# Kernel optimization log

Hardware: AMD Instinct MI355X
Metric: run time of the kernel (lower is better)

## Reference

```python
import jax, jax.numpy as jnp
import numpy as np

NUM_CODES = 100000
DIM = 64
N_VISITS = 16384
MAX_CODES = 64


def setup_inputs() -> dict:
    key = jax.random.key(0)
    k1, k2 = jax.random.split(key)
    # ids in [-5, NUM_CODES): negatives act as padding (original filters ids >= 0)
    code_ids = jax.random.randint(k1, (N_VISITS, MAX_CODES), -5, NUM_CODES, dtype=jnp.int64)
    emb_weight = jax.random.normal(k2, (NUM_CODES, DIM), dtype=jnp.float32)
    return {"code_ids": code_ids, "emb_weight": emb_weight}


def reference(code_ids, emb_weight):
    # mask of valid (non-negative) code ids per visit
    mask = code_ids >= 0                                  # [N, C] bool
    safe_ids = jnp.where(mask, code_ids, 0)               # clamp padding to 0 for gather
    x = emb_weight[safe_ids]                              # [N, C, D] gather
    maskf = mask.astype(emb_weight.dtype)
    sums = jnp.einsum('ncd,nc->nd', x, maskf)             # masked sum over codes
    counts = maskf.sum(axis=1, keepdims=True)             # [N, 1]
    # mean over valid ids; visits with zero valid ids -> zero vector
    out = sums / jnp.maximum(counts, 1.0)
    return jnp.where(counts > 0, out, 0.0)
```

## Files before the change

kernel.cpp:

```cpp
#include <hip/hip_runtime.h>

#define N_VISITS  16384
#define MAX_CODES 64
#define DIM       64

__global__ __launch_bounds__(256) void visit_mean_kernel(
    const int* __restrict__ code_ids,
    const float* __restrict__ emb,
    float* __restrict__ out)
{
    const int wave_in_block = threadIdx.x >> 6;
    const int lane = threadIdx.x & 63;
    const int visit = blockIdx.x * 4 + wave_in_block;
    if (visit >= N_VISITS) return;

    const int my_id = code_ids[visit * MAX_CODES + lane];

    const unsigned long long valid = __ballot(my_id >= 0);
    const int count = __popcll(valid);

    float sum = 0.0f;

    #pragma unroll
    for (int j0 = 0; j0 < MAX_CODES; j0 += 16) {
        float v[16];
        float m[16];
        #pragma unroll
        for (int k = 0; k < 16; ++k) {
            const int idj  = __shfl(my_id, j0 + k, 64);
            const int safe = (idj >= 0) ? idj : 0;
            m[k] = (idj >= 0) ? 1.0f : 0.0f;
            v[k] = emb[(size_t)safe * DIM + lane];
        }
        #pragma unroll
        for (int k = 0; k < 16; ++k) {
            sum = fmaf(m[k], v[k], sum);
        }
    }

    const float scale = (count > 0) ? (1.0f / (float)count) : 0.0f;
    out[visit * DIM + lane] = sum * scale;
}

extern "C" void kernel_launch(void* const* d_in, const int* in_sizes, int n_in,
                              void* d_out, int out_size, void* d_ws, size_t ws_size,
                              hipStream_t stream) {
    const int*   code_ids = (const int*)d_in[0];
    const float* emb      = (const float*)d_in[1];
    float*       out      = (float*)d_out;

    const int waves_per_block = 4;
    const int grid = N_VISITS / waves_per_block;
    visit_mean_kernel<<<grid, 256, 0, stream>>>(code_ids, emb, out);
}
```

Baseline: 100.9 us.

## Vectorize embedding gathers with float4 loads and cross-lane reduction

Each wave now processes four embedding rows at a time: lanes are split into four groups of 16, and each lane loads a float4 from its assigned row. Sixteen gathered rows per lane are accumulated, and the four partial sums are combined with xor shuffles before 16 lanes write float4 outputs. This replaces 64 scalar gather loads per lane with 16 wider loads, cutting the number of memory instructions and giving more loads in flight. The cost is more registers for the 16 float4 values and an added shuffle reduction stage. The bounds check on the visit index is also removed.

```diff
diff --git a/kernel.cpp b/kernel.cpp
--- a/kernel.cpp
+++ b/kernel.cpp
@@ -12,34 +12,56 @@
     const int wave_in_block = threadIdx.x >> 6;
     const int lane = threadIdx.x & 63;
     const int visit = blockIdx.x * 4 + wave_in_block;
-    if (visit >= N_VISITS) return;
 
-    const int my_id = code_ids[visit * MAX_CODES + lane];
+    const int r = lane >> 4;
+    const int t = lane & 15;
 
+    const int my_id = code_ids[(size_t)visit * MAX_CODES + lane];
     const unsigned long long valid = __ballot(my_id >= 0);
     const int count = __popcll(valid);
 
-    float sum = 0.0f;
-
+    int ids[16];
     #pragma unroll
-    for (int j0 = 0; j0 < MAX_CODES; j0 += 16) {
-        float v[16];
-        float m[16];
-        #pragma unroll
-        for (int k = 0; k < 16; ++k) {
-            const int idj  = __shfl(my_id, j0 + k, 64);
-            const int safe = (idj >= 0) ? idj : 0;
-            m[k] = (idj >= 0) ? 1.0f : 0.0f;
-            v[k] = emb[(size_t)safe * DIM + lane];
-        }
-        #pragma unroll
-        for (int k = 0; k < 16; ++k) {
-            sum = fmaf(m[k], v[k], sum);
-        }
+    for (int j = 0; j < 16; ++j) {
+        ids[j] = __shfl(my_id, 4 * j + r, 64);
     }
 
-    const float scale = (count > 0) ? (1.0f / (float)count) : 0.0f;
-    out[visit * DIM + lane] = sum * scale;
+    float4 v[16];
+    #pragma unroll
+    for (int j = 0; j < 16; ++j) {
+        const int id   = ids[j];
+        const int safe = (id >= 0) ? id : 0;
+        v[j] = *((const float4*)(emb + (size_t)safe * DIM) + t);
+    }
+
+    float4 acc = make_float4(0.f, 0.f, 0.f, 0.f);
+    #pragma unroll
+    for (int j = 0; j < 16; ++j) {
+        const float m = (ids[j] >= 0) ? 1.0f : 0.0f;
+        acc.x = fmaf(m, v[j].x, acc.x);
+        acc.y = fmaf(m, v[j].y, acc.y);
+        acc.z = fmaf(m, v[j].z, acc.z);
+        acc.w = fmaf(m, v[j].w, acc.w);
+    }
+
+    acc.x += __shfl_xor(acc.x, 16, 64);
+    acc.y += __shfl_xor(acc.y, 16, 64);
+    acc.z += __shfl_xor(acc.z, 16, 64);
+    acc.w += __shfl_xor(acc.w, 16, 64);
+    acc.x += __shfl_xor(acc.x, 32, 64);
+    acc.y += __shfl_xor(acc.y, 32, 64);
+    acc.z += __shfl_xor(acc.z, 32, 64);
+    acc.w += __shfl_xor(acc.w, 32, 64);
+
+    if (lane < 16) {
+        const float scale = (count > 0) ? (1.0f / (float)count) : 0.0f;
+        float4 o;
+        o.x = acc.x * scale;
+        o.y = acc.y * scale;
+        o.z = acc.z * scale;
+        o.w = acc.w * scale;
+        ((float4*)(out + (size_t)visit * DIM))[t] = o;
+    }
 }
 
 extern "C" void kernel_launch(void* const* d_in, const int* in_sizes, int n_in,
```

New measurement: 100.5 us. Within noise of the previous version (-0.4%).
